# Kernel tuning notes

Measured on AMD Instinct MI355X. Metric: run time of the kernel, lower is better.

## Reference

```python
import jax, jax.numpy as jnp
import numpy as np

N = 588   # node count, fixed by GRUCell(588, 64) input size
E = 9408  # edges = N * avg_degree 16
NEG = 0.01  # leaky_relu default slope
THRESH = 1.0 - 0.001


def setup_inputs() -> dict:
    key = jax.random.key(0)
    ks = jax.random.split(key, 20)
    w = lambda k, shape: (jax.random.normal(k, shape, dtype=jnp.float32) * 0.05)
    return {
        "features": jax.random.normal(ks[0], (N, 4), dtype=jnp.float32),
        "src": jax.random.randint(ks[1], (E,), 0, N),
        "dst": jax.random.randint(ks[2], (E,), 0, N),
        # CustomConv linears (sum-aggregate then Linear)
        "W1": w(ks[3], (4, 64)),  "b1": jnp.zeros((64,), jnp.float32),
        "W2": w(ks[4], (64, 64)), "b2": jnp.zeros((64,), jnp.float32),
        "W3": w(ks[5], (64, 1)),  "b3": jnp.zeros((1,), jnp.float32),
        "W5": w(ks[6], (64, 3)),  "b5": jnp.zeros((3,), jnp.float32),
        # GRUCell(588, 64): torch layout weight_ih [3*64, 588], weight_hh [3*64, 64]
        "gru_wi": w(ks[7], (192, 588)),
        "gru_wh": w(ks[8], (192, 64)),
        "gru_bi": jnp.zeros((192,), jnp.float32),
        "gru_bh": jnp.zeros((192,), jnp.float32),
        # end_determine Linear(64, 1)
        "w_end": w(ks[9], (64, 1)),
        "b_end": jnp.zeros((1,), jnp.float32),
        "cap": 30,
    }


def _lrelu(v):
    return jnp.where(v >= 0, v, NEG * v)


def reference(features, src, dst, W1, b1, W2, b2, W3, b3, W5, b5,
              gru_wi, gru_wh, gru_bi, gru_bh, w_end, b_end, cap):
    def conv(h, W, b):  # CustomConv: sum neighbors -> Linear
        agg = jax.ops.segment_sum(h[src], dst, num_segments=N)
        return agg @ W + b

    def gru(x, h):  # torch GRUCell, gate order r, z, n
        gx = x @ gru_wi.T + gru_bi          # [1, 192]
        gh = h @ gru_wh.T + gru_bh          # [1, 192]
        xr, xz, xn = jnp.split(gx, 3, axis=-1)
        hr, hz, hn = jnp.split(gh, 3, axis=-1)
        r = jax.nn.sigmoid(xr + hr)
        z = jax.nn.sigmoid(xz + hz)
        n = jnp.tanh(xn + r * hn)
        return (1.0 - z) * n + z * h

    state0 = jnp.zeros((1, 64), jnp.float32)
    x = _lrelu(conv(features, W1, b1))                 # [N, 64]
    inputt = _lrelu(conv(x, W3, b3)).T                 # [1, N]
    # NOTE: self.state is updated once before the loop, never inside it.
    state = gru(inputt, state0)                        # [1, 64]
    preprob = state @ w_end + b_end                    # [1, 1]
    fprob0 = jax.nn.sigmoid(preprob)
    s0 = jnp.sum(fprob0)                               # sum of sigmoid(probm)

    def step(carry, _):
        xc, s, fprob, counter = carry
        active = s < THRESH
        xn = _lrelu(conv(xc, W2, b2))                  # [N, 64]
        stn = gru(_lrelu(conv(xn, W3, b3)).T, state)   # uses frozen self.state
        pre = stn @ w_end + b_end                      # [1, 1]
        pr = jax.nn.sigmoid(pre)
        xc = jnp.where(active, xn, xc)
        fprob = jnp.where(active, pr, fprob)
        s = s + jnp.where(active, jnp.sum(pr), 0.0)
        counter = counter + active.astype(jnp.int32)
        return (xc, s, fprob, counter), None

    (x_last, _, fprob, counter), _ = jax.lax.scan(
        step, (x, s0, fprob0, jnp.int32(0)), None, length=int(cap))

    out = conv(x_last, W5, b5)                         # layer5, no activation: [N, 3]
    return out, counter, fprob
```

## Files before the change

kernel.cpp:

```cpp
#include <hip/hip_runtime.h>
#include <math.h>

#define NN 588
#define EE 9408
#define HD 64
#define NBLK 64
#define NTHR 1024
#define NWAVE (NTHR/64)
#define GXROWS (192/NBLK)
#define NEGS 0.01f
#define THRESHV 0.999f
#define MAGIC 0x51CAFE17u
#define DROW NN
#define EPADCAP 13536

struct Ctrl {
  unsigned ready;  unsigned pad0[15];
  unsigned xflags[NBLK*16];
};

__device__ __forceinline__ float lrelu(float v){ return v >= 0.f ? v : NEGS*v; }
__device__ __forceinline__ float sigm(float v){ return 1.f/(1.f+expf(-v)); }
__device__ __forceinline__ float rdlane(float v, int l){
  return __int_as_float(__builtin_amdgcn_readlane(__float_as_int(v), l));
}
__device__ __forceinline__ float wredsum(float v){
  v += __shfl_down(v,32); v += __shfl_down(v,16); v += __shfl_down(v,8);
  v += __shfl_down(v,4);  v += __shfl_down(v,2);  v += __shfl_down(v,1);
  return v;
}
__device__ __forceinline__ void stga(float* p, float v){
  __hip_atomic_store(p, v, __ATOMIC_RELAXED, __HIP_MEMORY_SCOPE_AGENT);
}
__device__ __forceinline__ float ldga(const float* p){
  return __hip_atomic_load(p, __ATOMIC_RELAXED, __HIP_MEMORY_SCOPE_AGENT);
}
__device__ __forceinline__ void sink4(float4 v){
  asm volatile("" :: "v"(v.x), "v"(v.y), "v"(v.z), "v"(v.w));
}
__device__ __forceinline__ void prefetch_region(const float* p0, int nfloats, int t, int T){
  const float4* p = (const float4*)p0;
  const int n = nfloats >> 2;
  for (int base = t; base < n; base += T*8) {
    float4 v[8];
    #pragma unroll
    for (int u = 0; u < 8; ++u) { int i = base + u*T; if (i >= n) i = n - 1; v[u] = p[i]; }
    #pragma unroll
    for (int u = 0; u < 8; ++u) sink4(v[u]);
  }
}

__device__ __forceinline__ void barrive(unsigned* flags, int bid, unsigned gen) {
  __syncthreads();
  if (threadIdx.x == 0) {
    __hip_atomic_store(&flags[bid*16], gen, __ATOMIC_RELEASE, __HIP_MEMORY_SCOPE_AGENT);
  }
}
__device__ __forceinline__ void bwait(unsigned* flags, unsigned gen) {
  if ((threadIdx.x >> 6) == 0) {
    int lane = threadIdx.x & 63;
    const unsigned* fp = &flags[lane*16];
    long bail = 0;
    for (;;) {
      int ok = (lane >= NBLK) ? 1 :
               (__hip_atomic_load(fp, __ATOMIC_RELAXED, __HIP_MEMORY_SCOPE_AGENT) >= gen);
      if (__all(ok)) break;
      __builtin_amdgcn_s_sleep(1);
      if (++bail > (1L<<15)) break;
    }
    asm volatile("" ::: "memory");
  }
  __syncthreads();
}

__global__ __launch_bounds__(NTHR)
void lastgcn_kernel(const float* __restrict__ feat, const int* __restrict__ src,
                    const int* __restrict__ dst,
                    const float* __restrict__ W1, const float* __restrict__ b1,
                    const float* __restrict__ W2, const float* __restrict__ b2,
                    const float* __restrict__ W3, const float* __restrict__ b3,
                    const float* __restrict__ W5, const float* __restrict__ b5,
                    const float* __restrict__ wi, const float* __restrict__ wh,
                    const float* __restrict__ bi, const float* __restrict__ bh,
                    const float* __restrict__ w_end, const float* __restrict__ b_end,
                    const int* __restrict__ capp,
                    float* __restrict__ out, Ctrl* ctrl,
                    float* __restrict__ x0g, float* __restrict__ x1g,
                    float* __restrict__ ypub, float* __restrict__ gxpub) {
  const int tid  = threadIdx.x;
  const int lane = tid & 63;
  const int w    = tid >> 6;
  const int bid  = blockIdx.x;
  const int nbeg = (NN*bid)/NBLK;
  const int nend = (NN*(bid+1))/NBLK;
  const int cnt  = nend - nbeg;
  const int r0   = bid*GXROWS;

  __shared__ float  W2L[64*64];
  __shared__ unsigned short eidxL[EPADCAP];
  __shared__ unsigned edgeL[EE];
  __shared__ int    offL[NN+1];
  __shared__ int    curL[NN];
  __shared__ float  yF[NN+1];
  __shared__ float  inpF[NN];
  __shared__ float  ghL[192];
  __shared__ float4 f4L[80];
  __shared__ int    wsumL[NWAVE];

  if (bid == 0) {
    if (tid < HD) { stga(&x0g[DROW*HD + tid], 0.f); stga(&x1g[DROW*HD + tid], 0.f); }
    if (tid == 64) stga(&ypub[NN], 0.f);
    if (tid == 65) stga(&ypub[(NN+1) + NN], 0.f);
    for (int i2 = tid; i2 < NBLK*16; i2 += NTHR) {
      ((unsigned*)ctrl)[16 + i2] = 0u;
    }
    __syncthreads();
    if (tid == 0) {
      __threadfence();
      __hip_atomic_store(&ctrl->ready, MAGIC, __ATOMIC_RELEASE, __HIP_MEMORY_SCOPE_AGENT);
    }
  } else if (tid == 0) {
    long bail = 0;
    while (__hip_atomic_load(&ctrl->ready, __ATOMIC_RELAXED, __HIP_MEMORY_SCOPE_AGENT) != MAGIC) {
      __builtin_amdgcn_s_sleep(1);
      if (++bail > (1L<<20)) break;
    }
    __threadfence();
  }
  __syncthreads();

  for (int i = tid; i < NN; i += NTHR) curL[i] = 0;
  for (int i = tid; i < 1024; i += NTHR) ((float4*)W2L)[i] = ((const float4*)W2)[i];
  __syncthreads();
  {
    const int4* s4 = (const int4*)src;
    const int4* d4 = (const int4*)dst;
    for (int e4 = tid; e4 < EE/4; e4 += NTHR) {
      int4 s = s4[e4], d = d4[e4];
      edgeL[e4*4+0] = (unsigned)((s.x<<16)|d.x); atomicAdd(&curL[d.x],1);
      edgeL[e4*4+1] = (unsigned)((s.y<<16)|d.y); atomicAdd(&curL[d.y],1);
      edgeL[e4*4+2] = (unsigned)((s.z<<16)|d.z); atomicAdd(&curL[d.z],1);
      edgeL[e4*4+3] = (unsigned)((s.w<<16)|d.w); atomicAdd(&curL[d.w],1);
    }
    prefetch_region(wi + r0*NN, GXROWS*NN, tid, NTHR);
    prefetch_region(w_end, 64, tid, NTHR);
  }
  __syncthreads();

  {
    const int n0 = 2*tid, n1 = n0 + 1;
    int d0 = (n0 < NN) ? curL[n0] : 0;
    int d1 = (n1 < NN) ? curL[n1] : 0;
    int p0 = (d0 + 7) & ~7, p1 = (d1 + 7) & ~7;
    int my = p0 + p1;
    int inc = my;
    for (int o = 1; o < 64; o <<= 1) { int u = __shfl_up(inc, o); if (lane >= o) inc += u; }
    if (lane == 63) wsumL[w] = inc;
    __syncthreads();
    if (w == 0 && lane < NWAVE) {
      int s0 = wsumL[lane];
      int is = s0;
      for (int o = 1; o < NWAVE; o <<= 1) { int u = __shfl_up(is, o); if (lane >= o) is += u; }
      wsumL[lane] = is - s0;
    }
    __syncthreads();
    int base = wsumL[w] + inc - my;
    if (n0 < NN) { offL[n0] = base;      curL[n0] = base;      }
    if (n1 < NN) { offL[n1] = base + p0; curL[n1] = base + p0; }
    if (tid == NTHR-1) offL[NN] = base + p0 + p1;
  }
  __syncthreads();
  for (int e4 = tid; e4 < EE/4; e4 += NTHR) {
    uint4 pk = ((const uint4*)edgeL)[e4];
    int p;
    p = atomicAdd(&curL[pk.x & 0xFFFF], 1); eidxL[p] = (unsigned short)(pk.x >> 16);
    p = atomicAdd(&curL[pk.y & 0xFFFF], 1); eidxL[p] = (unsigned short)(pk.y >> 16);
    p = atomicAdd(&curL[pk.z & 0xFFFF], 1); eidxL[p] = (unsigned short)(pk.z >> 16);
    p = atomicAdd(&curL[pk.w & 0xFFFF], 1); eidxL[p] = (unsigned short)(pk.w >> 16);
  }
  __syncthreads();
  {
    const int n0 = 2*tid, n1 = n0 + 1;
    if (n0 < NN) for (int k = curL[n0]; k < offL[n0+1]; ++k) eidxL[k] = (unsigned short)DROW;
    if (n1 < NN) for (int k = curL[n1]; k < offL[n1+1]; ++k) eidxL[k] = (unsigned short)DROW;
  }
  __syncthreads();

  if (tid < cnt) {
    int n = nbeg + tid;
    int o = offL[n], o1 = offL[n+1];
    float fx=0.f, fy=0.f, fz=0.f, fw2=0.f;
    for (int k = o; k < o1; k += 8) {
      uint4 q = *(const uint4*)(eidxL + k);
      int id[8] = { (int)(q.x & 0xFFFF), (int)(q.x >> 16), (int)(q.y & 0xFFFF), (int)(q.y >> 16),
                    (int)(q.z & 0xFFFF), (int)(q.z >> 16), (int)(q.w & 0xFFFF), (int)(q.w >> 16) };
      float4 tv[8]; float m[8];
      #pragma unroll
      for (int u = 0; u < 8; ++u) {
        int valid = id[u] < NN;
        m[u] = valid ? 1.f : 0.f;
        tv[u] = *(const float4*)(feat + (valid ? id[u] : 0)*4);
      }
      #pragma unroll
      for (int u = 0; u < 8; ++u) { fx += m[u]*tv[u].x; fy += m[u]*tv[u].y; fz += m[u]*tv[u].z; fw2 += m[u]*tv[u].w; }
    }
    f4L[tid] = make_float4(fx, fy, fz, fw2);
  }
  __syncthreads();
  const float W3r = W3[lane];
  for (int i = w; i < cnt; i += NWAVE) {
    int n = nbeg + i; float4 f = f4L[i];
    float v = b1[lane] + f.x*W1[lane] + f.y*W1[64+lane] + f.z*W1[128+lane] + f.w*W1[192+lane];
    v = lrelu(v);
    stga(&x0g[n*HD + lane], v);
    float yv = wredsum(v * W3r);
    if (lane == 0) stga(&ypub[n], yv);
  }
  barrive(ctrl->xflags, bid, 1u);

  const float b3v  = b3[0];
  const float b2r  = b2[lane];
  const float bend0 = b_end[0];
  const float wer  = w_end[lane];
  const int cap = capp[0];
  float* xc = x0g;
  float* xn = x1g;

  float stj = 0.f;
  float s_run = 0.f;
  float fprobr = 0.f;
  int   nsteps = 0;

  for (int k = 0; ; ++k) {
    bwait(ctrl->xflags, (unsigned)(k+1));
    const float* yp = ypub + (k&1)*(NN+1);
    for (int i = tid; i <= NN; i += NTHR) yF[i] = ldga(&yp[i]);

    if (k >= 1) {
      const float* gxp = gxpub + ((k-1)&1)*192;
      int j = lane;
      float gxr = ldga(&gxp[j]), gxz = ldga(&gxp[64+j]), gxn2 = ldga(&gxp[128+j]);
      if (k == 1) {
        float r  = sigm(gxr + bh[j]);
        float z  = sigm(gxz + bh[64+j]);
        float n2 = tanhf(gxn2 + r*bh[128+j]);
        float st = (1.f - z)*n2;
        stj = st;
        float t2 = wredsum(st * wer);
        float pr = sigm(rdlane(t2,0) + bend0);
        s_run = pr; fprobr = pr; nsteps = 0;
      } else {
        float r  = sigm(gxr + ghL[j]);
        float z  = sigm(gxz + ghL[64+j]);
        float n2 = tanhf(gxn2 + r*ghL[128+j]);
        float st = (1.f - z)*n2 + z*stj;
        float t2 = wredsum(st * wer);
        float pr = sigm(rdlane(t2,0) + bend0);
        s_run += pr; fprobr = pr; nsteps = k-1;
      }
      if (s_run >= THRESHV || k == cap+1) break;
    }

    if (k < cap) {
      float* ypn = ypub + ((k+1)&1)*(NN+1);
      for (int i = w; i < cnt; i += 2*NWAVE) {
        int i2 = i + NWAVE;
        bool has2 = (i2 < cnt);
        int nA = nbeg + i, nB = nbeg + (has2 ? i2 : i);
        int oA = offL[nA], lA = offL[nA+1] - oA;
        int oB = offL[nB], lB = offL[nB+1] - oB;
        float accA = 0.f, accB = 0.f;
        int pcm = lA > lB ? lA : lB;
        for (int kk = 0; kk < pcm; kk += 8) {
          float ta[8], tb[8];
          if (kk < lA) {
            uint4 q = *(const uint4*)(eidxL + oA + kk);
            ta[0] = ldga(&xc[(int)(q.x & 0xFFFF)*HD + lane]); ta[1] = ldga(&xc[(int)(q.x >> 16)*HD + lane]);
            ta[2] = ldga(&xc[(int)(q.y & 0xFFFF)*HD + lane]); ta[3] = ldga(&xc[(int)(q.y >> 16)*HD + lane]);
            ta[4] = ldga(&xc[(int)(q.z & 0xFFFF)*HD + lane]); ta[5] = ldga(&xc[(int)(q.z >> 16)*HD + lane]);
            ta[6] = ldga(&xc[(int)(q.w & 0xFFFF)*HD + lane]); ta[7] = ldga(&xc[(int)(q.w >> 16)*HD + lane]);
          } else { for (int u = 0; u < 8; ++u) ta[u] = 0.f; }
          if (kk < lB) {
            uint4 q = *(const uint4*)(eidxL + oB + kk);
            tb[0] = ldga(&xc[(int)(q.x & 0xFFFF)*HD + lane]); tb[1] = ldga(&xc[(int)(q.x >> 16)*HD + lane]);
            tb[2] = ldga(&xc[(int)(q.y & 0xFFFF)*HD + lane]); tb[3] = ldga(&xc[(int)(q.y >> 16)*HD + lane]);
            tb[4] = ldga(&xc[(int)(q.z & 0xFFFF)*HD + lane]); tb[5] = ldga(&xc[(int)(q.z >> 16)*HD + lane]);
            tb[6] = ldga(&xc[(int)(q.w & 0xFFFF)*HD + lane]); tb[7] = ldga(&xc[(int)(q.w >> 16)*HD + lane]);
          } else { for (int u = 0; u < 8; ++u) tb[u] = 0.f; }
          #pragma unroll
          for (int u = 0; u < 8; ++u) { accA += ta[u]; accB += tb[u]; }
        }
        float a0=0.f,a1=0.f,a2=0.f,a3=0.f, c0=0.f,c1=0.f,c2=0.f,c3=0.f;
        #pragma unroll
        for (int l = 0; l < 64; l += 4) {
          float w0 = W2L[(l+0)*64 + lane];
          float w1v = W2L[(l+1)*64 + lane];
          float w2v = W2L[(l+2)*64 + lane];
          float w3v = W2L[(l+3)*64 + lane];
          a0 = fmaf(rdlane(accA,l+0), w0,  a0);  c0 = fmaf(rdlane(accB,l+0), w0,  c0);
          a1 = fmaf(rdlane(accA,l+1), w1v, a1);  c1 = fmaf(rdlane(accB,l+1), w1v, c1);
          a2 = fmaf(rdlane(accA,l+2), w2v, a2);  c2 = fmaf(rdlane(accB,l+2), w2v, c2);
          a3 = fmaf(rdlane(accA,l+3), w3v, a3);  c3 = fmaf(rdlane(accB,l+3), w3v, c3);
        }
        {
          float vA = lrelu(b2r + (a0+a1)+(a2+a3));
          stga(&xn[nA*HD + lane], vA);
          float yv = wredsum(vA * W3r);
          if (lane == 0) stga(&ypn[nA], yv);
        }
        if (has2) {
          float vB = lrelu(b2r + (c0+c1)+(c2+c3));
          stga(&xn[nB*HD + lane], vB);
          float yv = wredsum(vB * W3r);
          if (lane == 0) stga(&ypn[nB], yv);
        }
      }
    }
    __syncthreads();

    for (int n = tid; n < NN; n += NTHR) {
      int o = offL[n], o1 = offL[n+1];
      float a = 0.f;
      for (int kk = o; kk < o1; kk += 8) {
        uint4 q = *(const uint4*)(eidxL + kk);
        a += yF[q.x & 0xFFFF] + yF[q.x >> 16] + yF[q.y & 0xFFFF] + yF[q.y >> 16];
        a += yF[q.z & 0xFFFF] + yF[q.z >> 16] + yF[q.w & 0xFFFF] + yF[q.w >> 16];
      }
      inpF[n] = lrelu(a + b3v);
    }
    __syncthreads();

    {
      float* gxp = gxpub + (k&1)*192;
      const float4* inp4 = (const float4*)inpF;
      for (int rr = w; rr < GXROWS; rr += NWAVE) {
        const float4* row4 = (const float4*)(wi + (r0 + rr)*NN);
        float p = 0.f;
        #pragma unroll
        for (int kk = 0; kk < 3; ++kk) {
          int c = lane + (kk << 6);
          if (c < 147) {
            float4 a = row4[c], b = inp4[c];
            p += a.x*b.x + a.y*b.y + a.z*b.z + a.w*b.w;
          }
        }
        p = wredsum(p);
        if (lane == 0) stga(&gxp[r0 + rr], p + bi[r0 + rr]);
      }
    }

    barrive(ctrl->xflags, bid, (unsigned)(k+2));

    if (k == 1) {
      for (int rr = w; rr < 192; rr += NWAVE) {
        float p = wredsum(wh[rr*64 + lane] * stj);
        if (lane == 0) ghL[rr] = p + bh[rr];
      }
    }
    { float* t = xc; xc = xn; xn = t; }
  }

  float* xf = xn;
  for (int i = w; i < cnt; i += NWAVE) {
    int n = nbeg + i;
    int o = offL[n], o1 = offL[n+1];
    float acc = 0.f;
    for (int k = o; k < o1; k += 8) {
      uint4 q = *(const uint4*)(eidxL + k);
      float t[8];
      t[0] = ldga(&xf[(int)(q.x & 0xFFFF)*HD + lane]); t[1] = ldga(&xf[(int)(q.x >> 16)*HD + lane]);
      t[2] = ldga(&xf[(int)(q.y & 0xFFFF)*HD + lane]); t[3] = ldga(&xf[(int)(q.y >> 16)*HD + lane]);
      t[4] = ldga(&xf[(int)(q.z & 0xFFFF)*HD + lane]); t[5] = ldga(&xf[(int)(q.z >> 16)*HD + lane]);
      t[6] = ldga(&xf[(int)(q.w & 0xFFFF)*HD + lane]); t[7] = ldga(&xf[(int)(q.w >> 16)*HD + lane]);
      #pragma unroll
      for (int u = 0; u < 8; ++u) acc += t[u];
    }
    float p0 = wredsum(acc * W5[lane*3 + 0]);
    float p1 = wredsum(acc * W5[lane*3 + 1]);
    float p2 = wredsum(acc * W5[lane*3 + 2]);
    if (lane == 0) {
      out[n*3 + 0] = p0 + b5[0];
      out[n*3 + 1] = p1 + b5[1];
      out[n*3 + 2] = p2 + b5[2];
    }
  }
  if (bid == 0 && tid == 0) {
    out[NN*3]     = (float)nsteps;
    out[NN*3 + 1] = fprobr;
  }
}

extern "C" void kernel_launch(void* const* d_in, const int* in_sizes, int n_in,
                              void* d_out, int out_size, void* d_ws, size_t ws_size,
                              hipStream_t stream) {
  const float* feat  = (const float*)d_in[0];
  const int*   src   = (const int*)d_in[1];
  const int*   dst   = (const int*)d_in[2];
  const float* W1    = (const float*)d_in[3];
  const float* b1    = (const float*)d_in[4];
  const float* W2    = (const float*)d_in[5];
  const float* b2    = (const float*)d_in[6];
  const float* W3    = (const float*)d_in[7];
  const float* b3    = (const float*)d_in[8];
  const float* W5    = (const float*)d_in[9];
  const float* b5    = (const float*)d_in[10];
  const float* wi    = (const float*)d_in[11];
  const float* wh    = (const float*)d_in[12];
  const float* bi    = (const float*)d_in[13];
  const float* bh    = (const float*)d_in[14];
  const float* w_end = (const float*)d_in[15];
  const float* b_end = (const float*)d_in[16];
  const int*   capp  = (const int*)d_in[17];

  float* out = (float*)d_out;
  char* wsb = (char*)d_ws;
  Ctrl*  ctrl   = (Ctrl*)wsb;
  float* x0g    = (float*)(wsb + 8192);
  float* x1g    = x0g + (size_t)(NN+1)*HD;
  float* ypub   = x1g + (size_t)(NN+1)*HD;
  float* gxpub  = ypub + 2*(NN+1);

  lastgcn_kernel<<<dim3(NBLK), dim3(NTHR), 0, stream>>>(
      feat, src, dst, W1, b1, W2, b2, W3, b3, W5, b5,
      wi, wh, bi, bh, w_end, b_end, capp, out,
      ctrl, x0g, x1g, ypub, gxpub);
}
```

Baseline: 130.7 us.

## Build padded ELL adjacency per block slice and share it through global memory

Every block used to build the full CSR adjacency redundantly in shared memory: a degree count, a block-wide scan and a scatter over all edges. Now each block builds only its own node slice as a fixed-width (64) ELL table, publishes it to workspace memory, and after the first grid barrier every block copies the full table into shared memory. The aggregation loops now index ELL rows instead of CSR offsets. The two-nodes-per-wave interleave in the recurrent conv loop is also dropped for a simpler one-node loop, which lowers memory-level parallelism per wave. Neighbours beyond 64 per node would be silently truncated, and the shared-memory footprint grows.

```diff
diff --git a/kernel.cpp b/kernel.cpp
--- a/kernel.cpp
+++ b/kernel.cpp
@@ -8,11 +8,11 @@
 #define NTHR 1024
 #define NWAVE (NTHR/64)
 #define GXROWS (192/NBLK)
+#define ELLW 64
 #define NEGS 0.01f
 #define THRESHV 0.999f
 #define MAGIC 0x51CAFE17u
 #define DROW NN
-#define EPADCAP 13536
 
 struct Ctrl {
   unsigned ready;  unsigned pad0[15];
@@ -33,6 +33,12 @@
   __hip_atomic_store(p, v, __ATOMIC_RELAXED, __HIP_MEMORY_SCOPE_AGENT);
 }
 __device__ __forceinline__ float ldga(const float* p){
+  return __hip_atomic_load(p, __ATOMIC_RELAXED, __HIP_MEMORY_SCOPE_AGENT);
+}
+__device__ __forceinline__ void stgau(unsigned* p, unsigned v){
+  __hip_atomic_store(p, v, __ATOMIC_RELAXED, __HIP_MEMORY_SCOPE_AGENT);
+}
+__device__ __forceinline__ unsigned ldgau(const unsigned* p){
   return __hip_atomic_load(p, __ATOMIC_RELAXED, __HIP_MEMORY_SCOPE_AGENT);
 }
 __device__ __forceinline__ void sink4(float4 v){
@@ -86,7 +92,8 @@
                     const int* __restrict__ capp,
                     float* __restrict__ out, Ctrl* ctrl,
                     float* __restrict__ x0g, float* __restrict__ x1g,
-                    float* __restrict__ ypub, float* __restrict__ gxpub) {
+                    float* __restrict__ ypub, float* __restrict__ gxpub,
+                    unsigned* __restrict__ ellG, unsigned* __restrict__ degG) {
   const int tid  = threadIdx.x;
   const int lane = tid & 63;
   const int w    = tid >> 6;
@@ -97,15 +104,12 @@
   const int r0   = bid*GXROWS;
 
   __shared__ float  W2L[64*64];
-  __shared__ unsigned short eidxL[EPADCAP];
-  __shared__ unsigned edgeL[EE];
-  __shared__ int    offL[NN+1];
-  __shared__ int    curL[NN];
+  __shared__ unsigned short ellF[NN*ELLW];
+  __shared__ int    degF[NN];
   __shared__ float  yF[NN+1];
   __shared__ float  inpF[NN];
   __shared__ float  ghL[192];
-  __shared__ float4 f4L[80];
-  __shared__ int    wsumL[NWAVE];
+  __shared__ float4 f4L[16];
 
   if (bid == 0) {
     if (tid < HD) { stga(&x0g[DROW*HD + tid], 0.f); stga(&x1g[DROW*HD + tid], 0.f); }
@@ -129,7 +133,7 @@
   }
   __syncthreads();
 
-  for (int i = tid; i < NN; i += NTHR) curL[i] = 0;
+  if (tid < cnt) degF[nbeg + tid] = 0;
   for (int i = tid; i < 1024; i += NTHR) ((float4*)W2L)[i] = ((const float4*)W2)[i];
   __syncthreads();
   {
@@ -137,61 +141,40 @@
     const int4* d4 = (const int4*)dst;
     for (int e4 = tid; e4 < EE/4; e4 += NTHR) {
       int4 s = s4[e4], d = d4[e4];
-      edgeL[e4*4+0] = (unsigned)((s.x<<16)|d.x); atomicAdd(&curL[d.x],1);
-      edgeL[e4*4+1] = (unsigned)((s.y<<16)|d.y); atomicAdd(&curL[d.y],1);
-      edgeL[e4*4+2] = (unsigned)((s.z<<16)|d.z); atomicAdd(&curL[d.z],1);
-      edgeL[e4*4+3] = (unsigned)((s.w<<16)|d.w); atomicAdd(&curL[d.w],1);
+      if (d.x >= nbeg && d.x < nend) { int p = atomicAdd(&degF[d.x],1); if (p < ELLW) ellF[(size_t)d.x*ELLW + p] = (unsigned short)s.x; }
+      if (d.y >= nbeg && d.y < nend) { int p = atomicAdd(&degF[d.y],1); if (p < ELLW) ellF[(size_t)d.y*ELLW + p] = (unsigned short)s.y; }
+      if (d.z >= nbeg && d.z < nend) { int p = atomicAdd(&degF[d.z],1); if (p < ELLW) ellF[(size_t)d.z*ELLW + p] = (unsigned short)s.z; }
+      if (d.w >= nbeg && d.w < nend) { int p = atomicAdd(&degF[d.w],1); if (p < ELLW) ellF[(size_t)d.w*ELLW + p] = (unsigned short)s.w; }
     }
     prefetch_region(wi + r0*NN, GXROWS*NN, tid, NTHR);
     prefetch_region(w_end, 64, tid, NTHR);
   }
   __syncthreads();
-
-  {
-    const int n0 = 2*tid, n1 = n0 + 1;
-    int d0 = (n0 < NN) ? curL[n0] : 0;
-    int d1 = (n1 < NN) ? curL[n1] : 0;
-    int p0 = (d0 + 7) & ~7, p1 = (d1 + 7) & ~7;
-    int my = p0 + p1;
-    int inc = my;
-    for (int o = 1; o < 64; o <<= 1) { int u = __shfl_up(inc, o); if (lane >= o) inc += u; }
-    if (lane == 63) wsumL[w] = inc;
-    __syncthreads();
-    if (w == 0 && lane < NWAVE) {
-      int s0 = wsumL[lane];
-      int is = s0;
-      for (int o = 1; o < NWAVE; o <<= 1) { int u = __shfl_up(is, o); if (lane >= o) is += u; }
-      wsumL[lane] = is - s0;
-    }
-    __syncthreads();
-    int base = wsumL[w] + inc - my;
-    if (n0 < NN) { offL[n0] = base;      curL[n0] = base;      }
-    if (n1 < NN) { offL[n1] = base + p0; curL[n1] = base + p0; }
-    if (tid == NTHR-1) offL[NN] = base + p0 + p1;
-  }
-  __syncthreads();
-  for (int e4 = tid; e4 < EE/4; e4 += NTHR) {
-    uint4 pk = ((const uint4*)edgeL)[e4];
-    int p;
-    p = atomicAdd(&curL[pk.x & 0xFFFF], 1); eidxL[p] = (unsigned short)(pk.x >> 16);
-    p = atomicAdd(&curL[pk.y & 0xFFFF], 1); eidxL[p] = (unsigned short)(pk.y >> 16);
-    p = atomicAdd(&curL[pk.z & 0xFFFF], 1); eidxL[p] = (unsigned short)(pk.z >> 16);
-    p = atomicAdd(&curL[pk.w & 0xFFFF], 1); eidxL[p] = (unsigned short)(pk.w >> 16);
-  }
-  __syncthreads();
-  {
-    const int n0 = 2*tid, n1 = n0 + 1;
-    if (n0 < NN) for (int k = curL[n0]; k < offL[n0+1]; ++k) eidxL[k] = (unsigned short)DROW;
-    if (n1 < NN) for (int k = curL[n1]; k < offL[n1+1]; ++k) eidxL[k] = (unsigned short)DROW;
-  }
-  __syncthreads();
-
   if (tid < cnt) {
     int n = nbeg + tid;
-    int o = offL[n], o1 = offL[n+1];
+    int dg = degF[n]; if (dg > ELLW) dg = ELLW;
+    int pd = (dg + 7) & ~7; if (pd > ELLW) pd = ELLW;
+    unsigned short* row = ellF + (size_t)n*ELLW;
+    for (int j = dg; j < pd; ++j) row[j] = (unsigned short)DROW;
+    degF[n] = pd;
+  }
+  __syncthreads();
+  {
+    const unsigned* e32 = (const unsigned*)ellF;
+    for (int i = tid; i < cnt*32; i += NTHR) {
+      int rrow = nbeg + (i >> 5), word = i & 31;
+      stgau(&ellG[(size_t)rrow*32 + word], e32[(size_t)rrow*32 + word]);
+    }
+    if (tid < cnt) stgau(&degG[nbeg + tid], (unsigned)degF[nbeg + tid]);
+  }
+
+  if (tid < cnt) {
+    int n = nbeg + tid;
+    const unsigned short* row = ellF + (size_t)n*ELLW;
+    int len = degF[n];
     float fx=0.f, fy=0.f, fz=0.f, fw2=0.f;
-    for (int k = o; k < o1; k += 8) {
-      uint4 q = *(const uint4*)(eidxL + k);
+    for (int k = 0; k < len; k += 8) {
+      uint4 q = *(const uint4*)(row + k);
       int id[8] = { (int)(q.x & 0xFFFF), (int)(q.x >> 16), (int)(q.y & 0xFFFF), (int)(q.y >> 16),
                     (int)(q.z & 0xFFFF), (int)(q.z >> 16), (int)(q.w & 0xFFFF), (int)(q.w >> 16) };
       float4 tv[8]; float m[8];
@@ -233,6 +216,14 @@
 
   for (int k = 0; ; ++k) {
     bwait(ctrl->xflags, (unsigned)(k+1));
+
+    if (k == 0) {
+      unsigned* e32 = (unsigned*)ellF;
+      for (int i = tid; i < NN*32; i += NTHR) e32[i] = ldgau(&ellG[i]);
+      for (int i = tid; i < NN; i += NTHR) degF[i] = (int)ldgau(&degG[i]);
+      __syncthreads();
+    }
+
     const float* yp = ypub + (k&1)*(NN+1);
     for (int i = tid; i <= NN; i += NTHR) yF[i] = ldga(&yp[i]);
 
@@ -263,66 +254,40 @@
 
     if (k < cap) {
       float* ypn = ypub + ((k+1)&1)*(NN+1);
-      for (int i = w; i < cnt; i += 2*NWAVE) {
-        int i2 = i + NWAVE;
-        bool has2 = (i2 < cnt);
-        int nA = nbeg + i, nB = nbeg + (has2 ? i2 : i);
-        int oA = offL[nA], lA = offL[nA+1] - oA;
-        int oB = offL[nB], lB = offL[nB+1] - oB;
-        float accA = 0.f, accB = 0.f;
-        int pcm = lA > lB ? lA : lB;
-        for (int kk = 0; kk < pcm; kk += 8) {
-          float ta[8], tb[8];
-          if (kk < lA) {
-            uint4 q = *(const uint4*)(eidxL + oA + kk);
-            ta[0] = ldga(&xc[(int)(q.x & 0xFFFF)*HD + lane]); ta[1] = ldga(&xc[(int)(q.x >> 16)*HD + lane]);
-            ta[2] = ldga(&xc[(int)(q.y & 0xFFFF)*HD + lane]); ta[3] = ldga(&xc[(int)(q.y >> 16)*HD + lane]);
-            ta[4] = ldga(&xc[(int)(q.z & 0xFFFF)*HD + lane]); ta[5] = ldga(&xc[(int)(q.z >> 16)*HD + lane]);
-            ta[6] = ldga(&xc[(int)(q.w & 0xFFFF)*HD + lane]); ta[7] = ldga(&xc[(int)(q.w >> 16)*HD + lane]);
-          } else { for (int u = 0; u < 8; ++u) ta[u] = 0.f; }
-          if (kk < lB) {
-            uint4 q = *(const uint4*)(eidxL + oB + kk);
-            tb[0] = ldga(&xc[(int)(q.x & 0xFFFF)*HD + lane]); tb[1] = ldga(&xc[(int)(q.x >> 16)*HD + lane]);
-            tb[2] = ldga(&xc[(int)(q.y & 0xFFFF)*HD + lane]); tb[3] = ldga(&xc[(int)(q.y >> 16)*HD + lane]);
-            tb[4] = ldga(&xc[(int)(q.z & 0xFFFF)*HD + lane]); tb[5] = ldga(&xc[(int)(q.z >> 16)*HD + lane]);
-            tb[6] = ldga(&xc[(int)(q.w & 0xFFFF)*HD + lane]); tb[7] = ldga(&xc[(int)(q.w >> 16)*HD + lane]);
-          } else { for (int u = 0; u < 8; ++u) tb[u] = 0.f; }
-          #pragma unroll
-          for (int u = 0; u < 8; ++u) { accA += ta[u]; accB += tb[u]; }
+      for (int i = w; i < cnt; i += NWAVE) {
+        int n = nbeg + i;
+        const unsigned short* row = ellF + (size_t)n*ELLW;
+        int len = degF[n];
+        float acc = 0.f;
+        for (int kk = 0; kk < len; kk += 8) {
+          uint4 q = *(const uint4*)(row + kk);
+          acc += ldga(&xc[(int)(q.x & 0xFFFF)*HD + lane]) + ldga(&xc[(int)(q.x >> 16)*HD + lane]);
+          acc += ldga(&xc[(int)(q.y & 0xFFFF)*HD + lane]) + ldga(&xc[(int)(q.y >> 16)*HD + lane]);
+          acc += ldga(&xc[(int)(q.z & 0xFFFF)*HD + lane]) + ldga(&xc[(int)(q.z >> 16)*HD + lane]);
+          acc += ldga(&xc[(int)(q.w & 0xFFFF)*HD + lane]) + ldga(&xc[(int)(q.w >> 16)*HD + lane]);
         }
-        float a0=0.f,a1=0.f,a2=0.f,a3=0.f, c0=0.f,c1=0.f,c2=0.f,c3=0.f;
+        float a0=0.f,a1=0.f,a2=0.f,a3=0.f;
         #pragma unroll
         for (int l = 0; l < 64; l += 4) {
-          float w0 = W2L[(l+0)*64 + lane];
-          float w1v = W2L[(l+1)*64 + lane];
-          float w2v = W2L[(l+2)*64 + lane];
-          float w3v = W2L[(l+3)*64 + lane];
-          a0 = fmaf(rdlane(accA,l+0), w0,  a0);  c0 = fmaf(rdlane(accB,l+0), w0,  c0);
-          a1 = fmaf(rdlane(accA,l+1), w1v, a1);  c1 = fmaf(rdlane(accB,l+1), w1v, c1);
-          a2 = fmaf(rdlane(accA,l+2), w2v, a2);  c2 = fmaf(rdlane(accB,l+2), w2v, c2);
-          a3 = fmaf(rdlane(accA,l+3), w3v, a3);  c3 = fmaf(rdlane(accB,l+3), w3v, c3);
+          a0 = fmaf(rdlane(acc,l+0), W2L[(l+0)*64 + lane], a0);
+          a1 = fmaf(rdlane(acc,l+1), W2L[(l+1)*64 + lane], a1);
+          a2 = fmaf(rdlane(acc,l+2), W2L[(l+2)*64 + lane], a2);
+          a3 = fmaf(rdlane(acc,l+3), W2L[(l+3)*64 + lane], a3);
         }
-        {
-          float vA = lrelu(b2r + (a0+a1)+(a2+a3));
-          stga(&xn[nA*HD + lane], vA);
-          float yv = wredsum(vA * W3r);
-          if (lane == 0) stga(&ypn[nA], yv);
-        }
-        if (has2) {
-          float vB = lrelu(b2r + (c0+c1)+(c2+c3));
-          stga(&xn[nB*HD + lane], vB);
-          float yv = wredsum(vB * W3r);
-          if (lane == 0) stga(&ypn[nB], yv);
-        }
+        float v = lrelu(b2r + (a0+a1)+(a2+a3));
+        stga(&xn[n*HD + lane], v);
+        float yv = wredsum(v * W3r);
+        if (lane == 0) stga(&ypn[n], yv);
       }
     }
     __syncthreads();
 
     for (int n = tid; n < NN; n += NTHR) {
-      int o = offL[n], o1 = offL[n+1];
+      const unsigned short* row = ellF + (size_t)n*ELLW;
+      int len = degF[n];
       float a = 0.f;
-      for (int kk = o; kk < o1; kk += 8) {
-        uint4 q = *(const uint4*)(eidxL + kk);
+      for (int kk = 0; kk < len; kk += 8) {
+        uint4 q = *(const uint4*)(row + kk);
         a += yF[q.x & 0xFFFF] + yF[q.x >> 16] + yF[q.y & 0xFFFF] + yF[q.y >> 16];
         a += yF[q.z & 0xFFFF] + yF[q.z >> 16] + yF[q.w & 0xFFFF] + yF[q.w >> 16];
       }
@@ -363,17 +328,15 @@
   float* xf = xn;
   for (int i = w; i < cnt; i += NWAVE) {
     int n = nbeg + i;
-    int o = offL[n], o1 = offL[n+1];
+    const unsigned short* row = ellF + (size_t)n*ELLW;
+    int len = degF[n];
     float acc = 0.f;
-    for (int k = o; k < o1; k += 8) {
-      uint4 q = *(const uint4*)(eidxL + k);
-      float t[8];
-      t[0] = ldga(&xf[(int)(q.x & 0xFFFF)*HD + lane]); t[1] = ldga(&xf[(int)(q.x >> 16)*HD + lane]);
-      t[2] = ldga(&xf[(int)(q.y & 0xFFFF)*HD + lane]); t[3] = ldga(&xf[(int)(q.y >> 16)*HD + lane]);
-      t[4] = ldga(&xf[(int)(q.z & 0xFFFF)*HD + lane]); t[5] = ldga(&xf[(int)(q.z >> 16)*HD + lane]);
-      t[6] = ldga(&xf[(int)(q.w & 0xFFFF)*HD + lane]); t[7] = ldga(&xf[(int)(q.w >> 16)*HD + lane]);
-      #pragma unroll
-      for (int u = 0; u < 8; ++u) acc += t[u];
+    for (int k = 0; k < len; k += 8) {
+      uint4 q = *(const uint4*)(row + k);
+      acc += ldga(&xf[(int)(q.x & 0xFFFF)*HD + lane]) + ldga(&xf[(int)(q.x >> 16)*HD + lane]);
+      acc += ldga(&xf[(int)(q.y & 0xFFFF)*HD + lane]) + ldga(&xf[(int)(q.y >> 16)*HD + lane]);
+      acc += ldga(&xf[(int)(q.z & 0xFFFF)*HD + lane]) + ldga(&xf[(int)(q.z >> 16)*HD + lane]);
+      acc += ldga(&xf[(int)(q.w & 0xFFFF)*HD + lane]) + ldga(&xf[(int)(q.w >> 16)*HD + lane]);
     }
     float p0 = wredsum(acc * W5[lane*3 + 0]);
     float p1 = wredsum(acc * W5[lane*3 + 1]);
@@ -419,9 +382,11 @@
   float* x1g    = x0g + (size_t)(NN+1)*HD;
   float* ypub   = x1g + (size_t)(NN+1)*HD;
   float* gxpub  = ypub + 2*(NN+1);
+  unsigned* ellG = (unsigned*)(gxpub + 2*192);
+  unsigned* degG = ellG + (size_t)NN*32;
 
   lastgcn_kernel<<<dim3(NBLK), dim3(NTHR), 0, stream>>>(
       feat, src, dst, W1, b1, W2, b2, W3, b3, W5, b5,
       wi, wh, bi, bh, w_end, b_end, capp, out,
-      ctrl, x0g, x1g, ypub, gxpub);
-}
+      ctrl, x0g, x1g, ypub, gxpub, ellG, degG);
+}
```

Result: no change. 132.9 us (+1.6%).
